# Optimization experiments

Measured on AMD Instinct MI355X. Metric: run time of the kernel, lower is better.

Reference implementation:

```python
import jax, jax.numpy as jnp
import numpy as np

H, FH, D = 8, 4, 64          # num_heads, focal_heads, att_size
HID = H * D                   # hidden_size = 512
B, S = 8, 512                 # batch, num_nodes
T_HOP, T_EDGE = 32, 16
SCALE = D ** -0.5


def setup_inputs() -> dict:
    key = jax.random.key(0)
    ks = jax.random.split(key, 24)
    f = lambda i, shape: jax.random.normal(ks[i], shape, jnp.float32)
    w = 1.0 / np.sqrt(HID)
    inp = {
        'q': f(0, (B, S, HID)), 'k': f(1, (B, S, HID)), 'v': f(2, (B, S, HID)),
        'query_hop_emb': f(3, (T_HOP, HID)) * 0.02,
        'query_edge_emb': f(4, (T_EDGE, HID)) * 0.02,
        'key_hop_emb': f(5, (T_HOP, HID)) * 0.02,
        'key_edge_emb': f(6, (T_EDGE, HID)) * 0.02,
        'value_hop_emb': f(7, (T_HOP, HID)) * 0.02,
        'value_edge_emb': f(8, (T_EDGE, HID)) * 0.02,
        'distance': jax.random.randint(ks[9], (B, S, S), 0, T_HOP),
        'edge_attr': jax.random.randint(ks[10], (B, S, S), 0, T_EDGE),
        # guarantee at least one unmasked key per query row to keep softmax finite
        'mask': jax.random.bernoulli(ks[11], 0.9, (B, S)).at[:, 0].set(True),
        'focal_mask': jax.random.bernoulli(ks[12], 0.5, (B, S, S)).at[:, :, 0].set(True),
        'Wq': f(13, (HID, H * D)) * w, 'bq': f(14, (H * D,)) * 0.01,
        'Wk': f(15, (HID, H * D)) * w, 'bk': f(16, (H * D,)) * 0.01,
        'Wv': f(17, (HID, H * D)) * w, 'bv': f(18, (H * D,)) * 0.01,
        'Wo': f(19, (H * D, HID)) * w, 'bo': f(20, (HID,)) * 0.01,
    }
    return inp


def _emb_scores(x, emb):
    # x: [B,H,S,D], emb: [T, H*D] -> per-head scores [B,H,S,T]
    e = emb.reshape(-1, H, D).transpose(1, 0, 2)  # [H,T,D]
    return jnp.einsum('bhsd,htd->bhst', x, e)


def _gather_last(scores, idx):
    # scores: [B,H,S,T], idx: [B,S,S] -> [B,H,S,S]
    idx_b = jnp.broadcast_to(idx[:, None], (B, H, S, S))
    return jnp.take_along_axis(scores, idx_b, axis=3)


def _scatter_add_last(attn, idx, T):
    # attn: [B,H,S,S], idx: [B,S,S] -> [B,H,S,T] accumulating attn weights
    idx_b = jnp.broadcast_to(idx[:, None], (B, H, S, S)).reshape(B * H * S, S)
    rows = jnp.arange(B * H * S)[:, None]
    flat = (rows * T + idx_b).reshape(-1)
    out = jnp.zeros((B * H * S * T,), attn.dtype).at[flat].add(attn.reshape(-1))
    return out.reshape(B, H, S, T)


def reference(q, k, v, query_hop_emb, query_edge_emb, key_hop_emb, key_edge_emb,
              value_hop_emb, value_edge_emb, distance, edge_attr, mask, focal_mask,
              Wq, bq, Wk, bk, Wv, bv, Wo, bo):
    qh = (q @ Wq + bq).reshape(B, S, H, D).transpose(0, 2, 1, 3)  # [B,H,S,D]
    kh = (k @ Wk + bk).reshape(B, S, H, D).transpose(0, 2, 1, 3)
    vh = (v @ Wv + bv).reshape(B, S, H, D).transpose(0, 2, 1, 3)

    spatial_bias = (_gather_last(_emb_scores(qh, query_hop_emb), distance)
                    + _gather_last(_emb_scores(kh, key_hop_emb), distance))
    edge_bias = (_gather_last(_emb_scores(qh, query_edge_emb), edge_attr)
                 + _gather_last(_emb_scores(kh, key_edge_emb), edge_attr))

    attn = (jnp.einsum('bhsd,bhtd->bhst', qh, kh) + spatial_bias + edge_bias) * SCALE

    GS = H - FH
    a1 = jnp.where(mask[:, None, None, :], attn[:, :GS], -jnp.inf)
    a2 = jnp.where(focal_mask[:, None], attn[:, GS:], -jnp.inf)
    attn = jax.nn.softmax(jnp.concatenate([a1, a2], axis=1), axis=3)

    vha = _scatter_add_last(attn, distance, T_HOP)   # [B,H,S,T_HOP]
    vea = _scatter_add_last(attn, edge_attr, T_EDGE)  # [B,H,S,T_EDGE]
    vh_emb = value_hop_emb.reshape(T_HOP, H, D).transpose(1, 0, 2)   # [H,T,D]
    ve_emb = value_edge_emb.reshape(T_EDGE, H, D).transpose(1, 0, 2)

    x = (jnp.einsum('bhst,bhtd->bhsd', attn, vh)
         + jnp.einsum('bhst,htd->bhsd', vha, vh_emb)
         + jnp.einsum('bhst,htd->bhsd', vea, ve_emb))
    x = x.transpose(0, 2, 1, 3).reshape(B, S, H * D)
    return x @ Wo + bo
```

## Files before the change

kernel.cpp:

```cpp
#include <hip/hip_runtime.h>

constexpr int nB = 8, nS = 512, nH = 8, nD = 64, nHID = 512;
constexpr int THOP = 32, TEDGE = 16;
constexpr float SCALE = 0.125f;
constexpr float NEGINF = -30000.0f;

typedef __attribute__((ext_vector_type(8))) short bf16x8;
typedef __attribute__((ext_vector_type(4))) float f32x4;

#define MFMA16(A, B, C) __builtin_amdgcn_mfma_f32_16x16x32_bf16(A, B, C, 0, 0, 0)

__device__ __align__(16) unsigned short g_qhi[(size_t)nB * nH * nS * nD];
__device__ __align__(16) unsigned short g_qlo[(size_t)nB * nH * nS * nD];
__device__ __align__(16) unsigned short g_khi[(size_t)nB * nH * nS * nD];
__device__ __align__(16) unsigned short g_klo[(size_t)nB * nH * nS * nD];
__device__ __align__(16) unsigned short g_vhiT[(size_t)nB * nH * nD * nS];
__device__ __align__(16) unsigned short g_vloT[(size_t)nB * nH * nD * nS];
__device__ __align__(16) unsigned short g_embh[96 * 512];
__device__ __align__(16) unsigned short g_embl[96 * 512];
__device__ __align__(16) unsigned short g_inhi[(size_t)3 * 2097152];
__device__ __align__(16) unsigned short g_inlo[(size_t)3 * 2097152];
__device__ __align__(16) unsigned short g_wth[(size_t)4 * 262144];
__device__ __align__(16) unsigned short g_wtl[(size_t)4 * 262144];
__device__ __align__(16) unsigned short g_xhi[(size_t)nB * nS * nHID];
__device__ __align__(16) unsigned short g_xlo[(size_t)nB * nS * nHID];
__device__ int g_flags[32];

__device__ __forceinline__ float ldf(const void* p, int isf32, size_t i) {
  if (isf32) return ((const float*)p)[i];
  unsigned int w = (unsigned int)(((const unsigned short*)p)[i]) << 16;
  return __uint_as_float(w);
}
__device__ __forceinline__ float bf2f(unsigned short h) {
  return __uint_as_float((unsigned)h << 16);
}
__device__ __forceinline__ float4 ldf4(const void* p, int isf32, size_t i) {
  if (isf32) return ((const float4*)p)[i >> 2];
  const ushort4 u = ((const ushort4*)p)[i >> 2];
  float4 r;
  r.x = bf2f(u.x); r.y = bf2f(u.y); r.z = bf2f(u.z); r.w = bf2f(u.w);
  return r;
}
__device__ __forceinline__ unsigned short f2bf(float x) {
  unsigned u = __float_as_uint(x);
  u += 0x7FFFu + ((u >> 16) & 1u);
  return (unsigned short)(u >> 16);
}

__device__ int detect_bool_mode(const unsigned char* p) {
  if (p[0] == 0x80 && p[1] == 0x3F) return 2;
  if (p[0] == 0x00 && p[1] == 0x3C) return 4;
  if (p[0] == 0x00 && p[3] == 0x3F) return 3;
  for (int i = 0; i < 64; i += 4)
    if (p[i + 1] | p[i + 2] | p[i + 3]) return 1;
  return 0;
}
__device__ __forceinline__ bool bool_at(const unsigned char* p, int mode, size_t i) {
  switch (mode) {
    case 0: return ((const int*)p)[i] != 0;
    case 1: return p[i] != 0;
    case 3: return ((const float*)p)[i] != 0.f;
    default: return ((const unsigned short*)p)[i] != 0;
  }
}

__global__ __launch_bounds__(256) void detect_all(
    const void* q, const void* k, const void* v,
    const void* qhe, const void* qee, const void* khe, const void* kee,
    const void* vhe, const void* vee,
    const int* dist, const int* edge,
    const unsigned char* mraw, const unsigned char* fraw,
    const void* Wq, const void* bq, const void* Wk, const void* bk,
    const void* Wv, const void* bv, const void* Wo, const void* bo) {
  __shared__ float sred[256];
  __shared__ int nzs;
  const int tid = threadIdx.x;
  const int blk = blockIdx.x;

  if (blk < 17) {
    const void* arrs[17] = {q, k, v, qhe, qee, khe, kee, vhe, vee,
                            Wq, bq, Wk, bk, Wv, bv, Wo, bo};
    const int full[17] = {2097152, 2097152, 2097152, 8192, 8192, 8192, 8192,
                          8192, 8192, 262144, 512, 262144, 512, 262144, 512,
                          262144, 512};
    const int n = full[blk] < 16384 ? full[blk] : 16384;
    const unsigned short* u = (const unsigned short*)arrs[blk];
    float m = 0.f;
    for (int i = tid; i < n; i += 256) {
      float x = __uint_as_float((unsigned int)u[i] << 16);
      if (x != x) x = 1e20f;
      m = fmaxf(m, fabsf(x));
    }
    sred[tid] = m;
    __syncthreads();
    for (int s = 128; s > 0; s >>= 1) {
      if (tid < s) sred[tid] = fmaxf(sred[tid], sred[tid + s]);
      __syncthreads();
    }
    if (tid == 0) g_flags[4 + blk] = (sred[0] > 1e3f) ? 1 : 0;
  } else if (blk == 17 || blk == 18) {
    const int* p = (blk == 17) ? dist : edge;
    if (tid == 0) nzs = 0;
    __syncthreads();
    int a = 0;
    for (int i = tid; i < 4096; i += 256) a |= p[2 * i + 1];
    if (a) atomicOr(&nzs, 1);
    __syncthreads();
    if (tid == 0) g_flags[blk - 17] = (nzs == 0);
  } else {
    if (tid == 0) {
      g_flags[2] = detect_bool_mode(mraw);
      g_flags[3] = detect_bool_mode(fraw);
    }
  }
}

__global__ __launch_bounds__(256) void emb_prep(
    const void* qhe, const void* khe, const void* qee, const void* kee) {
  const int blk = blockIdx.x;
  const void* srcs[4] = {qhe, khe, qee, kee};
  const int flagIdx[4] = {7, 9, 8, 10};
  const int counts[4] = {32 * 512, 32 * 512, 16 * 512, 16 * 512};
  const int dsts[4] = {0, 32 * 512, 64 * 512, 80 * 512};
  const int f = g_flags[flagIdx[blk]];
  const void* src = srcs[blk];
  const int n = counts[blk], d0 = dsts[blk];
  for (int i = threadIdx.x; i < n; i += 256) {
    const float x = ldf(src, f, i);
    const unsigned short hi = f2bf(x);
    g_embh[d0 + i] = hi;
    g_embl[d0 + i] = f2bf(x - bf2f(hi));
  }
}

__global__ __launch_bounds__(256) void split_prep(
    const void* q, const void* k, const void* v) {
  const int t = blockIdx.y;
  const void* srcs[3] = {q, k, v};
  const int f = g_flags[4 + t];
  const size_t base = (size_t)t * 2097152;
  const size_t i = ((size_t)blockIdx.x * 256 + threadIdx.x) * 4;
  const float4 v4 = ldf4(srcs[t], f, i);
  ushort4 h4, l4;
  h4.x = f2bf(v4.x); l4.x = f2bf(v4.x - bf2f(h4.x));
  h4.y = f2bf(v4.y); l4.y = f2bf(v4.y - bf2f(h4.y));
  h4.z = f2bf(v4.z); l4.z = f2bf(v4.z - bf2f(h4.z));
  h4.w = f2bf(v4.w); l4.w = f2bf(v4.w - bf2f(h4.w));
  *(ushort4*)&g_inhi[base + i] = h4;
  *(ushort4*)&g_inlo[base + i] = l4;
}

__global__ __launch_bounds__(256) void wt_prep(
    const void* Wq, const void* Wk, const void* Wv, const void* Wo) {
  __shared__ float t[64][65];
  const int mat = blockIdx.y;
  const void* srcs[4] = {Wq, Wk, Wv, Wo};
  const int fIdx[4] = {13, 15, 17, 19};
  const int f = g_flags[fIdx[mat]];
  const void* W = srcs[mat];
  const int k0 = (blockIdx.x >> 3) * 64, n0 = (blockIdx.x & 7) * 64;
  const int tid = threadIdx.x;
  const int r = tid >> 4, c4 = (tid & 15) * 4;
#pragma unroll
  for (int i = 0; i < 4; ++i) {
    const float4 v4 = ldf4(W, f, (size_t)(k0 + r + i * 16) * 512 + n0 + c4);
    t[r + i * 16][c4] = v4.x;
    t[r + i * 16][c4 + 1] = v4.y;
    t[r + i * 16][c4 + 2] = v4.z;
    t[r + i * 16][c4 + 3] = v4.w;
  }
  __syncthreads();
  unsigned short* dh = g_wth + (size_t)mat * 262144;
  unsigned short* dl = g_wtl + (size_t)mat * 262144;
#pragma unroll
  for (int i = 0; i < 4; ++i) {
    const int rn = r + i * 16;
    ushort4 h4, l4;
    const float v0 = t[c4][rn], v1 = t[c4 + 1][rn];
    const float v2 = t[c4 + 2][rn], v3 = t[c4 + 3][rn];
    h4.x = f2bf(v0); l4.x = f2bf(v0 - bf2f(h4.x));
    h4.y = f2bf(v1); l4.y = f2bf(v1 - bf2f(h4.y));
    h4.z = f2bf(v2); l4.z = f2bf(v2 - bf2f(h4.z));
    h4.w = f2bf(v3); l4.w = f2bf(v3 - bf2f(h4.w));
    *(ushort4*)&dh[(size_t)(n0 + rn) * 512 + k0 + c4] = h4;
    *(ushort4*)&dl[(size_t)(n0 + rn) * 512 + k0 + c4] = l4;
  }
}

__global__ __launch_bounds__(256) void gemm_mfma(
    const unsigned short* __restrict__ Ahi, const unsigned short* __restrict__ Alo,
    const unsigned short* __restrict__ Wth, const unsigned short* __restrict__ Wtl,
    const void* __restrict__ bias, int bFlag,
    float* __restrict__ dst, int mode) {
  __shared__ unsigned short As_hi[64][40];
  __shared__ unsigned short As_lo[64][40];
  __shared__ unsigned short Wt_hi[64][40];
  __shared__ unsigned short Wt_lo[64][40];
  const int bF = g_flags[bFlag];
  const int tid = threadIdx.x;
  const int m0 = blockIdx.y * 64, n0 = blockIdx.x * 64;
  const int w = tid >> 6, l = tid & 63, c = l & 15, g = l >> 4;
  const int wr = w >> 1, wc = w & 1;
  const int sr = tid >> 2, sc = (tid & 3) * 8;

  f32x4 acc[2][2] = {{{0.f, 0.f, 0.f, 0.f}, {0.f, 0.f, 0.f, 0.f}},
                     {{0.f, 0.f, 0.f, 0.f}, {0.f, 0.f, 0.f, 0.f}}};

  const size_t ga = (size_t)(m0 + sr) * 512 + sc;
  const size_t gw = (size_t)(n0 + sr) * 512 + sc;
  bf16x8 pa_h = *(const bf16x8*)(Ahi + ga);
  bf16x8 pa_l = *(const bf16x8*)(Alo + ga);
  bf16x8 pw_h = *(const bf16x8*)(Wth + gw);
  bf16x8 pw_l = *(const bf16x8*)(Wtl + gw);

  for (int k0 = 0; k0 < 512; k0 += 32) {
    __syncthreads();
    *(bf16x8*)&As_hi[sr][sc] = pa_h;
    *(bf16x8*)&As_lo[sr][sc] = pa_l;
    *(bf16x8*)&Wt_hi[sr][sc] = pw_h;
    *(bf16x8*)&Wt_lo[sr][sc] = pw_l;
    __syncthreads();
    if (k0 < 480) {
      pa_h = *(const bf16x8*)(Ahi + ga + k0 + 32);
      pa_l = *(const bf16x8*)(Alo + ga + k0 + 32);
      pw_h = *(const bf16x8*)(Wth + gw + k0 + 32);
      pw_l = *(const bf16x8*)(Wtl + gw + k0 + 32);
    }
#pragma unroll
    for (int mi = 0; mi < 2; ++mi) {
      const bf16x8 ah = *(const bf16x8*)&As_hi[wr * 32 + mi * 16 + c][g * 8];
      const bf16x8 al = *(const bf16x8*)&As_lo[wr * 32 + mi * 16 + c][g * 8];
#pragma unroll
      for (int nj = 0; nj < 2; ++nj) {
        const bf16x8 wh = *(const bf16x8*)&Wt_hi[wc * 32 + nj * 16 + c][g * 8];
        const bf16x8 wl = *(const bf16x8*)&Wt_lo[wc * 32 + nj * 16 + c][g * 8];
        acc[mi][nj] = MFMA16(ah, wh, acc[mi][nj]);
        acc[mi][nj] = MFMA16(al, wh, acc[mi][nj]);
        acc[mi][nj] = MFMA16(ah, wl, acc[mi][nj]);
      }
    }
  }
#pragma unroll
  for (int mi = 0; mi < 2; ++mi)
#pragma unroll
    for (int nj = 0; nj < 2; ++nj)
#pragma unroll
      for (int r = 0; r < 4; ++r) {
        const int m = m0 + wr * 32 + mi * 16 + 4 * g + r;
        const int n = n0 + wc * 32 + nj * 16 + c;
        const float v2 = acc[mi][nj][r] + ldf(bias, bF, n);
        if (mode == 3) {
          dst[(size_t)m * 512 + n] = v2;
        } else {
          const int b = m >> 9, s = m & 511, h = n >> 6, d = n & 63;
          const unsigned short hi = f2bf(v2);
          const unsigned short lo = f2bf(v2 - bf2f(hi));
          if (mode == 0) {
            const size_t i0 = (((size_t)(b * nH + h) * nS) + s) * nD + d;
            g_qhi[i0] = hi; g_qlo[i0] = lo;
          } else if (mode == 1) {
            const size_t i0 = (((size_t)(b * nH + h) * nS) + s) * nD + d;
            g_khi[i0] = hi; g_klo[i0] = lo;
          } else {
            const size_t i0 = (((size_t)(b * nH + h) * nD) + d) * nS + s;
            g_vhiT[i0] = hi; g_vloT[i0] = lo;
          }
        }
      }
}

__global__ __launch_bounds__(256) void attn_kernel(
    const int* __restrict__ dist, const int* __restrict__ edge,
    const unsigned char* __restrict__ mraw, const unsigned char* __restrict__ fraw,
    const void* __restrict__ vhe, const void* __restrict__ vee) {
  __shared__ unsigned short kvbuf[8192];
  __shared__ unsigned short plds[16][520];
  __shared__ float chop_s[16][33];
  __shared__ float cedge_s[16][17];
  __shared__ float vha_s[16][33];
  __shared__ float vea_s[16][17];
  __shared__ float red_s[16][4];
  __shared__ float red2_s[16][4];
  __shared__ float rinv_s[16];

  const int id = blockIdx.x;
  const int bh = (id & 7) * 8 + ((id >> 3) & 7);
  const int qt = id >> 6;
  const int b = bh >> 3, h = bh & 7;
  const int q0 = qt * 16;
  const int tid = threadIdx.x;
  const int w = tid >> 6, l = tid & 63, c = l & 15, g = l >> 4;

  const int d64 = g_flags[0], e64 = g_flags[1];
  const int mmode = g_flags[2], fmode = g_flags[3];
  const int fvhe = g_flags[11], fvee = g_flags[12];

  for (int i = tid; i < 16 * 33; i += 256) (&vha_s[0][0])[i] = 0.f;
  for (int i = tid; i < 16 * 17; i += 256) (&vea_s[0][0])[i] = 0.f;

  const size_t rowbase = ((size_t)b * nS + q0) * nS;
  for (int j4 = tid; j4 < 2048; j4 += 256) {
    const int j = j4 * 4, r = j >> 9, c1 = j & 511;
    int dv[4], ev[4];
    if (!d64) {
      const int4 t = ((const int4*)(dist + rowbase))[j4];
      dv[0] = t.x & 31; dv[1] = t.y & 31; dv[2] = t.z & 31; dv[3] = t.w & 31;
    } else {
      const int4 t0 = ((const int4*)(dist + 2 * rowbase))[2 * j4];
      const int4 t1 = ((const int4*)(dist + 2 * rowbase))[2 * j4 + 1];
      dv[0] = t0.x & 31; dv[1] = t0.z & 31; dv[2] = t1.x & 31; dv[3] = t1.z & 31;
    }
    if (!e64) {
      const int4 t = ((const int4*)(edge + rowbase))[j4];
      ev[0] = t.x & 15; ev[1] = t.y & 15; ev[2] = t.z & 15; ev[3] = t.w & 15;
    } else {
      const int4 t0 = ((const int4*)(edge + 2 * rowbase))[2 * j4];
      const int4 t1 = ((const int4*)(edge + 2 * rowbase))[2 * j4 + 1];
      ev[0] = t0.x & 15; ev[1] = t0.z & 15; ev[2] = t1.x & 15; ev[3] = t1.z & 15;
    }
    ushort4 pw;
    unsigned short* pp = (unsigned short*)&pw;
#pragma unroll
    for (int t = 0; t < 4; ++t) {
      const bool keep = (h < 4) ? bool_at(mraw, mmode, (size_t)b * nS + c1 + t)
                                : bool_at(fraw, fmode, rowbase + j + t);
      pp[t] = (unsigned short)(dv[t] | (ev[t] << 5) | ((int)keep << 9));
    }
    *(ushort4*)&plds[r][c1] = pw;
  }

  const size_t qbase = (((size_t)bh * nS) + q0 + c) * nD + g * 8;
  const bf16x8 qh0 = *(const bf16x8*)(g_qhi + qbase);
  const bf16x8 qh1 = *(const bf16x8*)(g_qhi + qbase + 32);
  const bf16x8 ql0 = *(const bf16x8*)(g_qlo + qbase);
  const bf16x8 ql1 = *(const bf16x8*)(g_qlo + qbase + 32);

  if (w < 3) {
    const bool isEdge = (w == 2);
    const int tb = (w == 1) ? 16 : 0;
    const size_t qe0 = (isEdge ? (size_t)64 * 512 : 0) + (size_t)(tb + c) * 512 + h * 64;
    const size_t ke0 = (isEdge ? (size_t)80 * 512 : (size_t)32 * 512) + (size_t)(tb + c) * 512 + h * 64;
    f32x4 acc = {0.f, 0.f, 0.f, 0.f};
#pragma unroll
    for (int dh = 0; dh < 2; ++dh) {
      const bf16x8 qhh = dh ? qh1 : qh0;
      const bf16x8 qll = dh ? ql1 : ql0;
      const bf16x8 khq = *(const bf16x8*)(g_khi + qbase + dh * 32);
      const bf16x8 klq = *(const bf16x8*)(g_klo + qbase + dh * 32);
      const bf16x8 eqh = *(const bf16x8*)(g_embh + qe0 + dh * 32 + g * 8);
      const bf16x8 eql = *(const bf16x8*)(g_embl + qe0 + dh * 32 + g * 8);
      const bf16x8 ekh = *(const bf16x8*)(g_embh + ke0 + dh * 32 + g * 8);
      const bf16x8 ekl = *(const bf16x8*)(g_embl + ke0 + dh * 32 + g * 8);
      acc = MFMA16(qhh, eqh, acc);
      acc = MFMA16(qll, eqh, acc);
      acc = MFMA16(qhh, eql, acc);
      acc = MFMA16(khq, ekh, acc);
      acc = MFMA16(klq, ekh, acc);
      acc = MFMA16(khq, ekl, acc);
    }
    if (!isEdge) {
#pragma unroll
      for (int r = 0; r < 4; ++r) chop_s[4 * g + r][tb + c] = acc[r];
    } else {
#pragma unroll
      for (int r = 0; r < 4; ++r) cedge_s[4 * g + r][c] = acc[r];
    }
  }

#pragma unroll
  for (int it = 0; it < 2; ++it) {
    const int e = (tid << 3) + (it << 11);
    const int r = e >> 6, d0 = e & 63;
    const size_t src = (((size_t)bh * nS) + r) * nD + d0;
    const int dsti = (r << 6) + ((((d0 >> 3) ^ (r & 7))) << 3);
    *(bf16x8*)&kvbuf[dsti] = *(const bf16x8*)(g_khi + src);
    *(bf16x8*)&kvbuf[4096 + dsti] = *(const bf16x8*)(g_klo + src);
  }
  __syncthreads();

  f32x4 pS[8];
  const int sw8 = c & 7;
  for (int ch = 0; ch < 8; ++ch) {
    const int rloc = w * 16 + c;
    const int a0 = rloc << 6;
    f32x4 acc = {0.f, 0.f, 0.f, 0.f};
    {
      const int o0 = a0 + ((g ^ sw8) << 3);
      const int o1 = a0 + ((((4 + g) ^ sw8)) << 3);
      const bf16x8 kh0 = *(const bf16x8*)&kvbuf[o0];
      const bf16x8 kl0 = *(const bf16x8*)&kvbuf[4096 + o0];
      const bf16x8 kh1 = *(const bf16x8*)&kvbuf[o1];
      const bf16x8 kl1 = *(const bf16x8*)&kvbuf[4096 + o1];
      acc = MFMA16(kh0, qh0, acc);
      acc = MFMA16(kl0, qh0, acc);
      acc = MFMA16(kh0, ql0, acc);
      acc = MFMA16(kh1, qh1, acc);
      acc = MFMA16(kl1, qh1, acc);
      acc = MFMA16(kh1, ql1, acc);
    }
    const int key0 = ch * 64 + w * 16 + 4 * g;
    const ushort4 pv4 = *(const ushort4*)&plds[c][key0];
    const unsigned short pp[4] = {pv4.x, pv4.y, pv4.z, pv4.w};
#pragma unroll
    for (int r = 0; r < 4; ++r) {
      const float s = (acc[r] + chop_s[c][pp[r] & 31] +
                       cedge_s[c][(pp[r] >> 5) & 15]) * SCALE;
      pS[ch][r] = (pp[r] & 512) ? s : NEGINF;
    }
    __syncthreads();
    if (ch < 7) {
#pragma unroll
      for (int it = 0; it < 2; ++it) {
        const int e = (tid << 3) + (it << 11);
        const int r = e >> 6, d0 = e & 63;
        const size_t src = (((size_t)bh * nS) + (ch + 1) * 64 + r) * nD + d0;
        const int dsti = (r << 6) + ((((d0 >> 3) ^ (r & 7))) << 3);
        *(bf16x8*)&kvbuf[dsti] = *(const bf16x8*)(g_khi + src);
        *(bf16x8*)&kvbuf[4096 + dsti] = *(const bf16x8*)(g_klo + src);
      }
      __syncthreads();
    }
  }

  float mx = NEGINF;
#pragma unroll
  for (int kt = 0; kt < 8; ++kt)
#pragma unroll
    for (int r = 0; r < 4; ++r) mx = fmaxf(mx, pS[kt][r]);
  mx = fmaxf(mx, __shfl_xor(mx, 16));
  mx = fmaxf(mx, __shfl_xor(mx, 32));
  if (l < 16) red_s[c][w] = mx;
  __syncthreads();
  const float M = fmaxf(fmaxf(red_s[c][0], red_s[c][1]),
                        fmaxf(red_s[c][2], red_s[c][3]));
  float sum = 0.f;
#pragma unroll
  for (int kt = 0; kt < 8; ++kt) {
    const int key0 = kt * 64 + w * 16 + 4 * g;
    const ushort4 pv4 = *(const ushort4*)&plds[c][key0];
    const unsigned short pp[4] = {pv4.x, pv4.y, pv4.z, pv4.w};
#pragma unroll
    for (int r = 0; r < 4; ++r) {
      const float pv = __expf(pS[kt][r] - M);
      pS[kt][r] = pv;
      sum += pv;
      atomicAdd(&vha_s[c][pp[r] & 31], pv);
      atomicAdd(&vea_s[c][(pp[r] >> 5) & 15], pv);
    }
  }
  sum += __shfl_xor(sum, 16);
  sum += __shfl_xor(sum, 32);
  if (l < 16) red2_s[c][w] = sum;
  int pk[8][2];
#pragma unroll
  for (int kt = 0; kt < 8; ++kt) {
    pk[kt][0] = ((int)f2bf(pS[kt][1]) << 16) | (int)f2bf(pS[kt][0]);
    pk[kt][1] = ((int)f2bf(pS[kt][3]) << 16) | (int)f2bf(pS[kt][2]);
  }
  __syncthreads();
  float (*x_s)[17] = reinterpret_cast<float(*)[17]>(&plds[0][0]);
  for (int i = tid; i < 64 * 17; i += 256) (&x_s[0][0])[i] = 0.f;
  if (w == 0 && l < 16) {
    const float tot = red2_s[c][0] + red2_s[c][1] + red2_s[c][2] + red2_s[c][3];
    rinv_s[c] = 1.0f / tot;
  }
  __syncthreads();

  f32x4 oacc[4] = {{0.f, 0.f, 0.f, 0.f}, {0.f, 0.f, 0.f, 0.f},
                   {0.f, 0.f, 0.f, 0.f}, {0.f, 0.f, 0.f, 0.f}};
  const int srcA = ((g & 1) * 2) * 16 + c;
  const int srcB = srcA + 16;
  const bool hi2 = (g >> 1) != 0;
  for (int p = 0; p < 4; ++p) {
#pragma unroll
    for (int it = 0; it < 4; ++it) {
      const int e = (tid << 3) + (it << 11);
      const int d = e >> 7, colc = e & 127;
      const size_t src = (((size_t)bh * nD) + d) * nS + (p << 7) + colc;
      const int dsti = (d << 7) + ((((colc >> 3) ^ (d & 15))) << 3);
      *(bf16x8*)&kvbuf[dsti] = *(const bf16x8*)(g_vhiT + src);
    }
    __syncthreads();
    const int t0d0 = __shfl(pk[2 * p][0], srcA);
    const int t1d0 = __shfl(pk[2 * p + 1][0], srcA);
    const int t0d1 = __shfl(pk[2 * p][1], srcA);
    const int t1d1 = __shfl(pk[2 * p + 1][1], srcA);
    const int t0d0b = __shfl(pk[2 * p][0], srcB);
    const int t1d0b = __shfl(pk[2 * p + 1][0], srcB);
    const int t0d1b = __shfl(pk[2 * p][1], srcB);
    const int t1d1b = __shfl(pk[2 * p + 1][1], srcB);
    union { int i[4]; bf16x8 v; } bu;
    bu.i[0] = hi2 ? t1d0 : t0d0;
    bu.i[1] = hi2 ? t1d1 : t0d1;
    bu.i[2] = hi2 ? t1d0b : t0d0b;
    bu.i[3] = hi2 ? t1d1b : t0d1b;
    const int col16 = (w << 1) + (g & 1) + ((g >> 1) << 3);
    const int j0 = (p << 7) + ((g >> 1) << 6) + (w << 4) + ((g & 1) << 3);
#pragma unroll
    for (int t = 0; t < 4; ++t) {
      const int row = t * 16 + c;
      const bf16x8 vh_ = *(const bf16x8*)&kvbuf[(row << 7) + (((col16 ^ c)) << 3)];
      const bf16x8 vl_ = *(const bf16x8*)(g_vloT + (((size_t)bh * nD) + row) * nS + j0);
      oacc[t] = MFMA16(vh_, bu.v, oacc[t]);
      oacc[t] = MFMA16(vl_, bu.v, oacc[t]);
    }
    __syncthreads();
  }
#pragma unroll
  for (int t = 0; t < 4; ++t)
#pragma unroll
    for (int r = 0; r < 4; ++r)
      atomicAdd(&x_s[t * 16 + 4 * g + r][c], oacc[t][r]);
  __syncthreads();

  {
    const int d = tid & 63, qq = tid >> 6;
    float val[4];
#pragma unroll
    for (int j = 0; j < 4; ++j) val[j] = x_s[d][qq + 4 * j];
    for (int t = 0; t < THOP; ++t) {
      const float e = ldf(vhe, fvhe, (size_t)t * nHID + h * 64 + d);
#pragma unroll
      for (int j = 0; j < 4; ++j) val[j] += vha_s[qq + 4 * j][t] * e;
    }
    for (int t = 0; t < TEDGE; ++t) {
      const float e = ldf(vee, fvee, (size_t)t * nHID + h * 64 + d);
#pragma unroll
      for (int j = 0; j < 4; ++j) val[j] += vea_s[qq + 4 * j][t] * e;
    }
#pragma unroll
    for (int j = 0; j < 4; ++j) {
      const int q = qq + 4 * j;
      const float xv = val[j] * rinv_s[q];
      const unsigned short hi = f2bf(xv);
      const size_t i0 = ((size_t)b * nS + q0 + q) * nHID + h * 64 + d;
      g_xhi[i0] = hi;
      g_xlo[i0] = f2bf(xv - bf2f(hi));
    }
  }
}

extern "C" void kernel_launch(void* const* d_in, const int* in_sizes, int n_in,
                              void* d_out, int out_size, void* d_ws, size_t ws_size,
                              hipStream_t stream) {
  const void* q   = d_in[0];
  const void* k   = d_in[1];
  const void* v   = d_in[2];
  const void* qhe = d_in[3];
  const void* qee = d_in[4];
  const void* khe = d_in[5];
  const void* kee = d_in[6];
  const void* vhe = d_in[7];
  const void* vee = d_in[8];
  const int* dist = (const int*)d_in[9];
  const int* edge = (const int*)d_in[10];
  const unsigned char* mraw = (const unsigned char*)d_in[11];
  const unsigned char* fraw = (const unsigned char*)d_in[12];
  const void* Wq = d_in[13];
  const void* bq = d_in[14];
  const void* Wk = d_in[15];
  const void* bk = d_in[16];
  const void* Wv = d_in[17];
  const void* bv = d_in[18];
  const void* Wo = d_in[19];
  const void* bo = d_in[20];

  detect_all<<<20, 256, 0, stream>>>(q, k, v, qhe, qee, khe, kee, vhe, vee,
                                     dist, edge, mraw, fraw,
                                     Wq, bq, Wk, bk, Wv, bv, Wo, bo);
  emb_prep<<<4, 256, 0, stream>>>(qhe, khe, qee, kee);
  split_prep<<<dim3(2048, 3), 256, 0, stream>>>(q, k, v);
  wt_prep<<<dim3(64, 4), 256, 0, stream>>>(Wq, Wk, Wv, Wo);

  unsigned short* inhi; hipGetSymbolAddress((void**)&inhi, HIP_SYMBOL(g_inhi));
  unsigned short* inlo; hipGetSymbolAddress((void**)&inlo, HIP_SYMBOL(g_inlo));
  unsigned short* wth;  hipGetSymbolAddress((void**)&wth,  HIP_SYMBOL(g_wth));
  unsigned short* wtl;  hipGetSymbolAddress((void**)&wtl,  HIP_SYMBOL(g_wtl));
  unsigned short* xhi;  hipGetSymbolAddress((void**)&xhi,  HIP_SYMBOL(g_xhi));
  unsigned short* xlo;  hipGetSymbolAddress((void**)&xlo,  HIP_SYMBOL(g_xlo));

  gemm_mfma<<<dim3(8, 64), 256, 0, stream>>>(inhi, inlo, wth, wtl,
                                             bq, 14, nullptr, 0);
  gemm_mfma<<<dim3(8, 64), 256, 0, stream>>>(inhi + 2097152, inlo + 2097152,
                                             wth + 262144, wtl + 262144,
                                             bk, 16, nullptr, 1);
  gemm_mfma<<<dim3(8, 64), 256, 0, stream>>>(inhi + 2 * 2097152, inlo + 2 * 2097152,
                                             wth + 2 * 262144, wtl + 2 * 262144,
                                             bv, 18, nullptr, 2);
  attn_kernel<<<2048, 256, 0, stream>>>(dist, edge, mraw, fraw, vhe, vee);
  gemm_mfma<<<dim3(8, 64), 256, 0, stream>>>(xhi, xlo,
                                             wth + 3 * 262144, wtl + 3 * 262144,
                                             bo, 20, (float*)d_out, 3);
}
```

Baseline: 649.1 us.

## Double-buffer K and V LDS staging in attention kernel to overlap loads

The single LDS staging buffer for K and V tiles becomes a two-slot buffer. The next K chunk or V panel is loaded while the current one feeds the MFMAs, which removes one barrier per iteration and lets global-memory latency overlap with compute. The first V panel is now issued before the softmax exponent pass. The change also adds a min-blocks-per-CU hint of 2 to the GEMM and attention kernels. The cost is 16 KB more LDS per block and higher register pressure from the hint, which may reduce occupancy or cause spills.

```diff
diff --git a/kernel.cpp b/kernel.cpp
--- a/kernel.cpp
+++ b/kernel.cpp
@@ -187,7 +187,7 @@
   }
 }
 
-__global__ __launch_bounds__(256) void gemm_mfma(
+__global__ __launch_bounds__(256, 2) void gemm_mfma(
     const unsigned short* __restrict__ Ahi, const unsigned short* __restrict__ Alo,
     const unsigned short* __restrict__ Wth, const unsigned short* __restrict__ Wtl,
     const void* __restrict__ bias, int bFlag,
@@ -269,11 +269,11 @@
       }
 }
 
-__global__ __launch_bounds__(256) void attn_kernel(
+__global__ __launch_bounds__(256, 2) void attn_kernel(
     const int* __restrict__ dist, const int* __restrict__ edge,
     const unsigned char* __restrict__ mraw, const unsigned char* __restrict__ fraw,
     const void* __restrict__ vhe, const void* __restrict__ vee) {
-  __shared__ unsigned short kvbuf[8192];
+  __shared__ unsigned short kvbuf[2][8192];
   __shared__ unsigned short plds[16][520];
   __shared__ float chop_s[16][33];
   __shared__ float cedge_s[16][17];
@@ -297,6 +297,28 @@
 
   for (int i = tid; i < 16 * 33; i += 256) (&vha_s[0][0])[i] = 0.f;
   for (int i = tid; i < 16 * 17; i += 256) (&vea_s[0][0])[i] = 0.f;
+
+  auto stageK = [&](int ch, int buf) {
+#pragma unroll
+    for (int it = 0; it < 2; ++it) {
+      const int e = (tid << 3) + (it << 11);
+      const int r = e >> 6, d0 = e & 63;
+      const size_t src = (((size_t)bh * nS) + ch * 64 + r) * nD + d0;
+      const int dsti = (r << 6) + (((d0 >> 3) ^ (r & 7)) << 3);
+      *(bf16x8*)&kvbuf[buf][dsti] = *(const bf16x8*)(g_khi + src);
+      *(bf16x8*)&kvbuf[buf][4096 + dsti] = *(const bf16x8*)(g_klo + src);
+    }
+  };
+  auto stageV = [&](int p, int buf) {
+#pragma unroll
+    for (int it = 0; it < 4; ++it) {
+      const int e = (tid << 3) + (it << 11);
+      const int d = e >> 7, colc = e & 127;
+      const size_t src = (((size_t)bh * nD) + d) * nS + (p << 7) + colc;
+      const int dsti = (d << 7) + (((colc >> 3) ^ (d & 15)) << 3);
+      *(bf16x8*)&kvbuf[buf][dsti] = *(const bf16x8*)(g_vhiT + src);
+    }
+  };
 
   const size_t rowbase = ((size_t)b * nS + q0) * nS;
   for (int j4 = tid; j4 < 2048; j4 += 256) {
@@ -367,30 +389,23 @@
     }
   }
 
-#pragma unroll
-  for (int it = 0; it < 2; ++it) {
-    const int e = (tid << 3) + (it << 11);
-    const int r = e >> 6, d0 = e & 63;
-    const size_t src = (((size_t)bh * nS) + r) * nD + d0;
-    const int dsti = (r << 6) + ((((d0 >> 3) ^ (r & 7))) << 3);
-    *(bf16x8*)&kvbuf[dsti] = *(const bf16x8*)(g_khi + src);
-    *(bf16x8*)&kvbuf[4096 + dsti] = *(const bf16x8*)(g_klo + src);
-  }
+  stageK(0, 0);
   __syncthreads();
 
   f32x4 pS[8];
   const int sw8 = c & 7;
   for (int ch = 0; ch < 8; ++ch) {
-    const int rloc = w * 16 + c;
-    const int a0 = rloc << 6;
+    if (ch < 7) stageK(ch + 1, (ch + 1) & 1);
+    const unsigned short* kb_ = kvbuf[ch & 1];
+    const int a0 = (w * 16 + c) << 6;
     f32x4 acc = {0.f, 0.f, 0.f, 0.f};
     {
       const int o0 = a0 + ((g ^ sw8) << 3);
-      const int o1 = a0 + ((((4 + g) ^ sw8)) << 3);
-      const bf16x8 kh0 = *(const bf16x8*)&kvbuf[o0];
-      const bf16x8 kl0 = *(const bf16x8*)&kvbuf[4096 + o0];
-      const bf16x8 kh1 = *(const bf16x8*)&kvbuf[o1];
-      const bf16x8 kl1 = *(const bf16x8*)&kvbuf[4096 + o1];
+      const int o1 = a0 + (((4 + g) ^ sw8) << 3);
+      const bf16x8 kh0 = *(const bf16x8*)&kb_[o0];
+      const bf16x8 kl0 = *(const bf16x8*)&kb_[4096 + o0];
+      const bf16x8 kh1 = *(const bf16x8*)&kb_[o1];
+      const bf16x8 kl1 = *(const bf16x8*)&kb_[4096 + o1];
       acc = MFMA16(kh0, qh0, acc);
       acc = MFMA16(kl0, qh0, acc);
       acc = MFMA16(kh0, ql0, acc);
@@ -408,18 +423,6 @@
       pS[ch][r] = (pp[r] & 512) ? s : NEGINF;
     }
     __syncthreads();
-    if (ch < 7) {
-#pragma unroll
-      for (int it = 0; it < 2; ++it) {
-        const int e = (tid << 3) + (it << 11);
-        const int r = e >> 6, d0 = e & 63;
-        const size_t src = (((size_t)bh * nS) + (ch + 1) * 64 + r) * nD + d0;
-        const int dsti = (r << 6) + ((((d0 >> 3) ^ (r & 7))) << 3);
-        *(bf16x8*)&kvbuf[dsti] = *(const bf16x8*)(g_khi + src);
-        *(bf16x8*)&kvbuf[4096 + dsti] = *(const bf16x8*)(g_klo + src);
-      }
-      __syncthreads();
-    }
   }
 
   float mx = NEGINF;
@@ -431,6 +434,7 @@
   mx = fmaxf(mx, __shfl_xor(mx, 32));
   if (l < 16) red_s[c][w] = mx;
   __syncthreads();
+  stageV(0, 0);
   const float M = fmaxf(fmaxf(red_s[c][0], red_s[c][1]),
                         fmaxf(red_s[c][2], red_s[c][3]));
   float sum = 0.f;
@@ -472,15 +476,8 @@
   const int srcB = srcA + 16;
   const bool hi2 = (g >> 1) != 0;
   for (int p = 0; p < 4; ++p) {
-#pragma unroll
-    for (int it = 0; it < 4; ++it) {
-      const int e = (tid << 3) + (it << 11);
-      const int d = e >> 7, colc = e & 127;
-      const size_t src = (((size_t)bh * nD) + d) * nS + (p << 7) + colc;
-      const int dsti = (d << 7) + ((((colc >> 3) ^ (d & 15))) << 3);
-      *(bf16x8*)&kvbuf[dsti] = *(const bf16x8*)(g_vhiT + src);
-    }
-    __syncthreads();
+    if (p < 3) stageV(p + 1, (p + 1) & 1);
+    const unsigned short* vb_ = kvbuf[p & 1];
     const int t0d0 = __shfl(pk[2 * p][0], srcA);
     const int t1d0 = __shfl(pk[2 * p + 1][0], srcA);
     const int t0d1 = __shfl(pk[2 * p][1], srcA);
@@ -499,7 +496,7 @@
 #pragma unroll
     for (int t = 0; t < 4; ++t) {
       const int row = t * 16 + c;
-      const bf16x8 vh_ = *(const bf16x8*)&kvbuf[(row << 7) + (((col16 ^ c)) << 3)];
+      const bf16x8 vh_ = *(const bf16x8*)&vb_[(row << 7) + ((col16 ^ c) << 3)];
       const bf16x8 vl_ = *(const bf16x8*)(g_vloT + (((size_t)bh * nD) + row) * nS + j0);
       oacc[t] = MFMA16(vh_, bu.v, oacc[t]);
       oacc[t] = MFMA16(vl_, bu.v, oacc[t]);
```

Measured after the change: 555.1 us. -14.5%, faster.

## Merge QKV GEMMs into one launch and stage V tiles earlier in attention

Applied to the files above, without the earlier changes.

The three Q/K/V projection GEMMs become a single launch with a 192-row grid, and the GEMM body is templated on its output mode. In the attention kernel, K and V staging move into helper lambdas, and the first V tile is now loaded before the softmax-reduction barrier so that load overlaps the reduction. Later V tiles are staged after each chunk's compute. Launch bounds ask for 4 blocks per CU, which may force register spilling. The aim is to cut launch overhead, fill the GPU better during the projections, and hide V load latency.

```diff
diff --git a/kernel.cpp b/kernel.cpp
--- a/kernel.cpp
+++ b/kernel.cpp
@@ -187,18 +187,16 @@
   }
 }
 
-__global__ __launch_bounds__(256) void gemm_mfma(
-    const unsigned short* __restrict__ Ahi, const unsigned short* __restrict__ Alo,
-    const unsigned short* __restrict__ Wth, const unsigned short* __restrict__ Wtl,
-    const void* __restrict__ bias, int bFlag,
-    float* __restrict__ dst, int mode) {
+template <int MODE_SEL>
+__device__ __forceinline__ void gemm_body(
+    const unsigned short* Ahi, const unsigned short* Alo,
+    const unsigned short* Wth, const unsigned short* Wtl,
+    const void* bias, int bF, float* dst, int mode, int m0, int n0) {
   __shared__ unsigned short As_hi[64][40];
   __shared__ unsigned short As_lo[64][40];
   __shared__ unsigned short Wt_hi[64][40];
   __shared__ unsigned short Wt_lo[64][40];
-  const int bF = g_flags[bFlag];
   const int tid = threadIdx.x;
-  const int m0 = blockIdx.y * 64, n0 = blockIdx.x * 64;
   const int w = tid >> 6, l = tid & 63, c = l & 15, g = l >> 4;
   const int wr = w >> 1, wc = w & 1;
   const int sr = tid >> 2, sc = (tid & 3) * 8;
@@ -249,7 +247,7 @@
         const int m = m0 + wr * 32 + mi * 16 + 4 * g + r;
         const int n = n0 + wc * 32 + nj * 16 + c;
         const float v2 = acc[mi][nj][r] + ldf(bias, bF, n);
-        if (mode == 3) {
+        if (MODE_SEL == 3) {
           dst[(size_t)m * 512 + n] = v2;
         } else {
           const int b = m >> 9, s = m & 511, h = n >> 6, d = n & 63;
@@ -269,7 +267,29 @@
       }
 }
 
-__global__ __launch_bounds__(256) void attn_kernel(
+__global__ __launch_bounds__(256, 4) void gemm_qkv(
+    const unsigned short* __restrict__ inhi, const unsigned short* __restrict__ inlo,
+    const unsigned short* __restrict__ wth, const unsigned short* __restrict__ wtl,
+    const void* __restrict__ bq, const void* __restrict__ bk,
+    const void* __restrict__ bv) {
+  const int mat = blockIdx.y >> 6;
+  const int m0 = (blockIdx.y & 63) * 64, n0 = blockIdx.x * 64;
+  const void* bias = (mat == 0) ? bq : (mat == 1) ? bk : bv;
+  const int bF = g_flags[14 + 2 * mat];
+  gemm_body<0>(inhi + (size_t)mat * 2097152, inlo + (size_t)mat * 2097152,
+               wth + (size_t)mat * 262144, wtl + (size_t)mat * 262144,
+               bias, bF, nullptr, mat, m0, n0);
+}
+
+__global__ __launch_bounds__(256, 4) void gemm_out(
+    const unsigned short* __restrict__ Ahi, const unsigned short* __restrict__ Alo,
+    const unsigned short* __restrict__ Wth, const unsigned short* __restrict__ Wtl,
+    const void* __restrict__ bias, float* __restrict__ dst) {
+  gemm_body<3>(Ahi, Alo, Wth, Wtl, bias, g_flags[20], dst, 3,
+               blockIdx.y * 64, blockIdx.x * 64);
+}
+
+__global__ __launch_bounds__(256, 4) void attn_kernel(
     const int* __restrict__ dist, const int* __restrict__ edge,
     const unsigned char* __restrict__ mraw, const unsigned char* __restrict__ fraw,
     const void* __restrict__ vhe, const void* __restrict__ vee) {
@@ -297,6 +317,28 @@
 
   for (int i = tid; i < 16 * 33; i += 256) (&vha_s[0][0])[i] = 0.f;
   for (int i = tid; i < 16 * 17; i += 256) (&vea_s[0][0])[i] = 0.f;
+
+  auto stageK = [&](int ch) {
+#pragma unroll
+    for (int it = 0; it < 2; ++it) {
+      const int e = (tid << 3) + (it << 11);
+      const int r = e >> 6, d0 = e & 63;
+      const size_t src = (((size_t)bh * nS) + ch * 64 + r) * nD + d0;
+      const int dsti = (r << 6) + (((d0 >> 3) ^ (r & 7)) << 3);
+      *(bf16x8*)&kvbuf[dsti] = *(const bf16x8*)(g_khi + src);
+      *(bf16x8*)&kvbuf[4096 + dsti] = *(const bf16x8*)(g_klo + src);
+    }
+  };
+  auto stageV = [&](int p) {
+#pragma unroll
+    for (int it = 0; it < 4; ++it) {
+      const int e = (tid << 3) + (it << 11);
+      const int d = e >> 7, colc = e & 127;
+      const size_t src = (((size_t)bh * nD) + d) * nS + (p << 7) + colc;
+      const int dsti = (d << 7) + (((colc >> 3) ^ (d & 15)) << 3);
+      *(bf16x8*)&kvbuf[dsti] = *(const bf16x8*)(g_vhiT + src);
+    }
+  };
 
   const size_t rowbase = ((size_t)b * nS + q0) * nS;
   for (int j4 = tid; j4 < 2048; j4 += 256) {
@@ -367,26 +409,17 @@
     }
   }
 
-#pragma unroll
-  for (int it = 0; it < 2; ++it) {
-    const int e = (tid << 3) + (it << 11);
-    const int r = e >> 6, d0 = e & 63;
-    const size_t src = (((size_t)bh * nS) + r) * nD + d0;
-    const int dsti = (r << 6) + ((((d0 >> 3) ^ (r & 7))) << 3);
-    *(bf16x8*)&kvbuf[dsti] = *(const bf16x8*)(g_khi + src);
-    *(bf16x8*)&kvbuf[4096 + dsti] = *(const bf16x8*)(g_klo + src);
-  }
+  stageK(0);
   __syncthreads();
 
   f32x4 pS[8];
   const int sw8 = c & 7;
   for (int ch = 0; ch < 8; ++ch) {
-    const int rloc = w * 16 + c;
-    const int a0 = rloc << 6;
+    const int a0 = (w * 16 + c) << 6;
     f32x4 acc = {0.f, 0.f, 0.f, 0.f};
     {
       const int o0 = a0 + ((g ^ sw8) << 3);
-      const int o1 = a0 + ((((4 + g) ^ sw8)) << 3);
+      const int o1 = a0 + (((4 + g) ^ sw8) << 3);
       const bf16x8 kh0 = *(const bf16x8*)&kvbuf[o0];
       const bf16x8 kl0 = *(const bf16x8*)&kvbuf[4096 + o0];
       const bf16x8 kh1 = *(const bf16x8*)&kvbuf[o1];
@@ -409,15 +442,7 @@
     }
     __syncthreads();
     if (ch < 7) {
-#pragma unroll
-      for (int it = 0; it < 2; ++it) {
-        const int e = (tid << 3) + (it << 11);
-        const int r = e >> 6, d0 = e & 63;
-        const size_t src = (((size_t)bh * nS) + (ch + 1) * 64 + r) * nD + d0;
-        const int dsti = (r << 6) + ((((d0 >> 3) ^ (r & 7))) << 3);
-        *(bf16x8*)&kvbuf[dsti] = *(const bf16x8*)(g_khi + src);
-        *(bf16x8*)&kvbuf[4096 + dsti] = *(const bf16x8*)(g_klo + src);
-      }
+      stageK(ch + 1);
       __syncthreads();
     }
   }
@@ -430,6 +455,7 @@
   mx = fmaxf(mx, __shfl_xor(mx, 16));
   mx = fmaxf(mx, __shfl_xor(mx, 32));
   if (l < 16) red_s[c][w] = mx;
+  stageV(0);
   __syncthreads();
   const float M = fmaxf(fmaxf(red_s[c][0], red_s[c][1]),
                         fmaxf(red_s[c][2], red_s[c][3]));
@@ -472,15 +498,6 @@
   const int srcB = srcA + 16;
   const bool hi2 = (g >> 1) != 0;
   for (int p = 0; p < 4; ++p) {
-#pragma unroll
-    for (int it = 0; it < 4; ++it) {
-      const int e = (tid << 3) + (it << 11);
-      const int d = e >> 7, colc = e & 127;
-      const size_t src = (((size_t)bh * nD) + d) * nS + (p << 7) + colc;
-      const int dsti = (d << 7) + ((((colc >> 3) ^ (d & 15))) << 3);
-      *(bf16x8*)&kvbuf[dsti] = *(const bf16x8*)(g_vhiT + src);
-    }
-    __syncthreads();
     const int t0d0 = __shfl(pk[2 * p][0], srcA);
     const int t1d0 = __shfl(pk[2 * p + 1][0], srcA);
     const int t0d1 = __shfl(pk[2 * p][1], srcA);
@@ -499,12 +516,16 @@
 #pragma unroll
     for (int t = 0; t < 4; ++t) {
       const int row = t * 16 + c;
-      const bf16x8 vh_ = *(const bf16x8*)&kvbuf[(row << 7) + (((col16 ^ c)) << 3)];
+      const bf16x8 vh_ = *(const bf16x8*)&kvbuf[(row << 7) + ((col16 ^ c) << 3)];
       const bf16x8 vl_ = *(const bf16x8*)(g_vloT + (((size_t)bh * nD) + row) * nS + j0);
       oacc[t] = MFMA16(vh_, bu.v, oacc[t]);
       oacc[t] = MFMA16(vl_, bu.v, oacc[t]);
     }
     __syncthreads();
+    if (p < 3) {
+      stageV(p + 1);
+      __syncthreads();
+    }
   }
 #pragma unroll
   for (int t = 0; t < 4; ++t)
@@ -579,16 +600,9 @@
   unsigned short* xhi;  hipGetSymbolAddress((void**)&xhi,  HIP_SYMBOL(g_xhi));
   unsigned short* xlo;  hipGetSymbolAddress((void**)&xlo,  HIP_SYMBOL(g_xlo));
 
-  gemm_mfma<<<dim3(8, 64), 256, 0, stream>>>(inhi, inlo, wth, wtl,
-                                             bq, 14, nullptr, 0);
-  gemm_mfma<<<dim3(8, 64), 256, 0, stream>>>(inhi + 2097152, inlo + 2097152,
-                                             wth + 262144, wtl + 262144,
-                                             bk, 16, nullptr, 1);
-  gemm_mfma<<<dim3(8, 64), 256, 0, stream>>>(inhi + 2 * 2097152, inlo + 2 * 2097152,
-                                             wth + 2 * 262144, wtl + 2 * 262144,
-                                             bv, 18, nullptr, 2);
+  gemm_qkv<<<dim3(8, 192), 256, 0, stream>>>(inhi, inlo, wth, wtl, bq, bk, bv);
   attn_kernel<<<2048, 256, 0, stream>>>(dist, edge, mraw, fraw, vhe, vee);
-  gemm_mfma<<<dim3(8, 64), 256, 0, stream>>>(xhi, xlo,
-                                             wth + 3 * 262144, wtl + 3 * 262144,
-                                             bo, 20, (float*)d_out, 3);
-}
+  gemm_out<<<dim3(8, 64), 256, 0, stream>>>(xhi, xlo,
+                                            wth + 3 * 262144, wtl + 3 * 262144,
+                                            bo, (float*)d_out);
+}
```

After: 609.9 us. -6.0%, faster.
